# Kernel optimization log

Hardware: AMD Instinct MI355X
Metric: run time of the kernel (lower is better)

Reference implementation:

```python
import jax, jax.numpy as jnp
import numpy as np

NUM_CLASSES = 19
PROJ_DIM = 128
QUEUE_LEN = 2975
B, H, W = 8, 128, 128
EPS = 1e-12  # torch F.normalize eps


def setup_inputs() -> dict:
    key = jax.random.key(0)
    k0, k1, k2, k3, k4 = jax.random.split(key, 5)
    proj3 = jax.random.normal(k0, (B, PROJ_DIM, H, W), jnp.float32)
    proj4 = jax.random.normal(k1, (B, PROJ_DIM, H, W), jnp.float32)
    proj5 = jax.random.normal(k2, (B, PROJ_DIM, H, W), jnp.float32)
    logits = jax.random.normal(k3, (B, NUM_CLASSES, H, W), jnp.float32)
    q = jax.random.normal(k4, (3, NUM_CLASSES, PROJ_DIM, QUEUE_LEN), jnp.float32)
    # buffers are L2-normalized along proj_dim at init
    queues = q / jnp.maximum(jnp.linalg.norm(q, axis=2, keepdims=True), EPS)
    return {"proj3": proj3, "proj4": proj4, "proj5": proj5,
            "logits": logits, "queues": queues}


def _region_keys(fea, pred):
    """fea: (D, HW) float, pred: (HW,) int. Masked mean per class, L2-normalized."""
    onehot = (pred[None, :] == jnp.arange(NUM_CLASSES)[:, None]).astype(fea.dtype)  # (C, HW)
    counts = onehot.sum(1)                                   # (C,)
    sums = jnp.einsum('ch,dh->cd', onehot, fea)              # (C, D)
    present = counts > 0
    means = sums / jnp.maximum(counts, 1.0)[:, None]
    keys = means / jnp.maximum(jnp.linalg.norm(means, axis=1, keepdims=True), EPS)
    return keys, present


def _contrast_loss(keys, present, queue):
    """keys: (C, D), queue: (C, D, L) (detached in original). Sum over present classes."""
    q = jax.lax.stop_gradient(queue)
    # (query . queue_col) implemented as elementwise-mul + mean over D in the original
    sim = jnp.einsum('cd,kdl->ckl', keys, q) / PROJ_DIM      # (C, C, L)
    ar = jnp.arange(NUM_CLASSES)
    pos = sim[ar, ar, :]                                     # (C, L)  l_pos per class
    exp_all = jnp.exp(sim)
    s_neg = exp_all.sum(axis=(1, 2)) - exp_all[ar, ar, :].sum(1)  # scalar neg mass per class
    loss_c = -(pos - jnp.log(jnp.exp(pos) + s_neg[:, None])).sum(1) / QUEUE_LEN
    return jnp.where(present, loss_c, 0.0).sum()


def _enqueue(queue, ptr, keys, present):
    """Write key into queue column ptr[c] for present classes, advance ptr by 1."""
    ar = jnp.arange(NUM_CLASSES)
    cur = queue[ar, :, ptr]                                  # (C, D)
    newcol = jnp.where(present[:, None], jax.lax.stop_gradient(keys), cur)
    queue = queue.at[ar, :, ptr].set(newcol)
    ptr = jnp.where(present, (ptr + 1) % QUEUE_LEN, ptr)
    return queue, ptr


def reference(proj3, proj4, proj5, logits, queues):
    pred = jnp.argmax(logits, axis=1).reshape(B, -1)         # (B, HW)
    total = jnp.float32(0.0)
    for pi, projector in enumerate((proj3, proj4, proj5)):
        fea_all = projector.reshape(B, PROJ_DIM, -1)          # (B, D, HW)

        def step(carry, inp):
            queue, ptr, acc = carry
            f, p = inp
            keys, present = _region_keys(f, p)
            acc = acc + _contrast_loss(keys, present, queue)
            queue, ptr = _enqueue(queue, ptr, keys, present)
            return (queue, ptr, acc), None

        init = (queues[pi], jnp.zeros((NUM_CLASSES,), jnp.int32), jnp.float32(0.0))
        (_, _, acc), _ = jax.lax.scan(step, init, (fea_all, pred))
        total = total + acc / B
    return total
```

## Files before the change

### kernel.cpp

```cpp
#include <hip/hip_runtime.h>
#include <stdint.h>

#define NCLS 19
#define PDIM 128
#define QLEN 2975
#define BATCH 8
#define HW 16384
#define ROWS 152
#define ROWS_PAD 160
#define HCHUNK 512

typedef __attribute__((ext_vector_type(8))) short short8;
typedef __attribute__((ext_vector_type(4))) float floatx4;

__device__ __forceinline__ uint16_t f2b(float f) {
    uint32_t u = __float_as_uint(f);
    uint32_t r = (u + 0x7FFFu + ((u >> 16) & 1u)) >> 16;
    return (uint16_t)r;
}

__global__ __launch_bounds__(256)
void k_pred(const float* __restrict__ logits, uint8_t* __restrict__ pred,
            int* __restrict__ counts) {
    __shared__ int cnt[NCLS];
    int tid = threadIdx.x;
    if (tid < NCLS) cnt[tid] = 0;
    __syncthreads();
    int idx = blockIdx.x * 256 + tid;
    int b = idx >> 14, h = idx & (HW - 1);
    const float* base = logits + (size_t)b * NCLS * HW + h;
    float best = base[0];
    int bi = 0;
#pragma unroll
    for (int c = 1; c < NCLS; ++c) {
        float v = base[(size_t)c * HW];
        if (v > best) { best = v; bi = c; }
    }
    pred[idx] = (uint8_t)bi;
    atomicAdd(&cnt[bi], 1);
    __syncthreads();
    if (tid < NCLS) atomicAdd(&counts[b * NCLS + tid], cnt[tid]);
}

__global__ __launch_bounds__(512)
void k_msum(const float* __restrict__ p0, const float* __restrict__ p1,
            const float* __restrict__ p2, const uint8_t* __restrict__ pred,
            float* __restrict__ sums) {
    int chunk = blockIdx.x, b = blockIdx.y, pi = blockIdx.z;
    const float* proj = (pi == 0) ? p0 : (pi == 1) ? p1 : p2;
    int tid = threadIdx.x;
    int wave = tid >> 6, lane = tid & 63;
    int col = lane & 15, g = lane >> 4;
    int d = wave * 16 + col;
    int h0 = chunk * HCHUNK;

    const float* frow = proj + ((size_t)b * PDIM + d) * HW;
    const uint8_t* pr = pred + (size_t)b * HW + h0;

    floatx4 acc0 = (floatx4)(0.f);
    floatx4 acc1 = (floatx4)(0.f);

#pragma unroll 4
    for (int s = 0; s < HCHUNK / 32; ++s) {
        int hk = h0 + s * 32 + g * 8;
        union { float4 f; uint4 u; } va, vb;
        va.f = *(const float4*)(frow + hk);
        vb.f = *(const float4*)(frow + hk + 4);
        uint64_t pb = *(const uint64_t*)(pr + s * 32 + g * 8);

        union { short8 s8; uint32_t w[4]; } bf;
        bf.w[0] = __builtin_amdgcn_perm(va.u.y, va.u.x, 0x07060302u);
        bf.w[1] = __builtin_amdgcn_perm(va.u.w, va.u.z, 0x07060302u);
        bf.w[2] = __builtin_amdgcn_perm(vb.u.y, vb.u.x, 0x07060302u);
        bf.w[3] = __builtin_amdgcn_perm(vb.u.w, vb.u.z, 0x07060302u);

        union { short8 s8; uint16_t h[8]; } a0, a1;
#pragma unroll
        for (int j = 0; j < 8; ++j) {
            int cb = (int)((pb >> (8 * j)) & 0xFF);
            a0.h[j] = (cb == col)      ? (uint16_t)0x3F80 : (uint16_t)0;
            a1.h[j] = (cb == col + 16) ? (uint16_t)0x3F80 : (uint16_t)0;
        }
        acc0 = __builtin_amdgcn_mfma_f32_16x16x32_bf16(a0.s8, bf.s8, acc0, 0, 0, 0);
        acc1 = __builtin_amdgcn_mfma_f32_16x16x32_bf16(a1.s8, bf.s8, acc1, 0, 0, 0);
    }

    float* sb = sums + (((size_t)pi * BATCH + b) * NCLS) * PDIM + d;
#pragma unroll
    for (int r = 0; r < 4; ++r) {
        int row0 = g * 4 + r;
        atomicAdd(&sb[(size_t)row0 * PDIM], acc0[r]);
        int row1 = 16 + g * 4 + r;
        if (row1 < NCLS) atomicAdd(&sb[(size_t)row1 * PDIM], acc1[r]);
    }
}

__global__ __launch_bounds__(64)
void k_keys(const float* __restrict__ sums, const int* __restrict__ counts,
            uint16_t* __restrict__ keysb) {
    int c = blockIdx.x, b = blockIdx.y, pi = blockIdx.z;
    int lane = threadIdx.x;
    size_t base = (((size_t)pi * BATCH + b) * NCLS + c) * PDIM;
    int cn = counts[b * NCLS + c];
    float cnt = (float)(cn > 0 ? cn : 1);
    float m0 = sums[base + lane] / cnt;
    float m1 = sums[base + lane + 64] / cnt;
    float nr = m0 * m0 + m1 * m1;
    for (int off = 32; off; off >>= 1) nr += __shfl_xor(nr, off);
    float scale = 1.f / fmaxf(sqrtf(nr), 1e-12f);
    size_t bb = ((size_t)pi * ROWS_PAD + b * NCLS + c) * PDIM;
    keysb[bb + lane]      = f2b(m0 * scale);
    keysb[bb + lane + 64] = f2b(m1 * scale);
}

__global__ __launch_bounds__(256, 2)
void k_sim(const float* __restrict__ q, const uint16_t* __restrict__ keysb,
           float* __restrict__ Sall, float* __restrict__ D0,
           float* __restrict__ pos0) {
    __shared__ char smem[40960];
    int tile = blockIdx.x, k = blockIdx.y, pi = blockIdx.z;
    int tid = threadIdx.x;
    int wave = tid >> 6, lane = tid & 63;
    int col = lane & 15, g = lane >> 4;

    {
        const uint4* kg = (const uint4*)(keysb + (size_t)pi * ROWS_PAD * PDIM);
        uint4* kl = (uint4*)smem;
        int kgrp = tid & 15;
        int r0 = tid >> 4;
#pragma unroll
        for (int it = 0; it < 10; ++it) {
            int row = r0 + it * 16;
            kl[kgrp * 160 + (row ^ (kgrp & 7))] = kg[row * 16 + kgrp];
        }
    }

    int l0 = tile * 128 + wave * 16 + col;
    int l1 = l0 + 64;
    bool okA = l0 < QLEN, okB = l1 < QLEN;
    const uint32_t* qbase = (const uint32_t*)(q + ((size_t)pi * NCLS + k) * (size_t)PDIM * QLEN);
    const uint32_t* qA = qbase + (okA ? l0 : (QLEN - 1));
    const uint32_t* qB = qbase + (okB ? l1 : (QLEN - 1));

    uint32_t uA[32], uB[32];
#pragma unroll
    for (int s = 0; s < 4; ++s) {
#pragma unroll
        for (int j = 0; j < 8; ++j) {
            size_t off = (size_t)(s * 32 + g * 8 + j) * QLEN;
            uA[s * 8 + j] = qA[off];
            uB[s * 8 + j] = qB[off];
        }
    }

    __syncthreads();

    uint32_t wA[16], wB[16];
#pragma unroll
    for (int t = 0; t < 16; ++t) {
        wA[t] = __builtin_amdgcn_perm(uA[2 * t + 1], uA[2 * t], 0x07060302u);
        wB[t] = __builtin_amdgcn_perm(uB[2 * t + 1], uB[2 * t], 0x07060302u);
    }

    floatx4 accA[10], accB[10];
#pragma unroll
    for (int m = 0; m < 10; ++m) { accA[m] = (floatx4)(0.f); accB[m] = (floatx4)(0.f); }

    const short8* kls = (const short8*)smem;
#pragma unroll
    for (int s = 0; s < 4; ++s) {
        union { short8 s8; uint32_t w[4]; } bfA, bfB;
#pragma unroll
        for (int i = 0; i < 4; ++i) { bfA.w[i] = wA[s * 4 + i]; bfB.w[i] = wB[s * 4 + i]; }
        int kgrp = s * 4 + g;
        int kxor = kgrp & 7;
        const short8* kp = kls + (size_t)kgrp * 160;
#pragma unroll
        for (int m = 0; m < 10; ++m) {
            short8 af = kp[(m * 16 + col) ^ kxor];
            accA[m] = __builtin_amdgcn_mfma_f32_16x16x32_bf16(af, bfA.s8, accA[m], 0, 0, 0);
            accB[m] = __builtin_amdgcn_mfma_f32_16x16x32_bf16(af, bfB.s8, accB[m], 0, 0, 0);
        }
    }

    __syncthreads();
    float* rowsum = (float*)smem;
    if (tid < ROWS_PAD) rowsum[tid] = 0.f;
    __syncthreads();

    const float inv = 1.f / (float)PDIM;
#pragma unroll
    for (int m = 0; m < 10; ++m) {
#pragma unroll
        for (int r = 0; r < 4; ++r) {
            int row = m * 16 + g * 4 + r;
            bool rok = row < ROWS;
            float sA = accA[m][r] * inv;
            float sB = accB[m][r] * inv;
            float e = 0.f;
            if (rok) e = (okA ? __expf(sA) : 0.f) + (okB ? __expf(sB) : 0.f);
#pragma unroll
            for (int off = 1; off < 16; off <<= 1) e += __shfl_xor(e, off);
            if (col == 0 && rok) atomicAdd(&rowsum[row], e);
            if (rok) {
                int bb = row / NCLS, cc = row - bb * NCLS;
                if (cc == k) {
                    float* pb = pos0 + (((size_t)pi * BATCH + bb) * NCLS + cc) * QLEN;
                    if (okA) pb[l0] = sA;
                    if (okB) pb[l1] = sB;
                }
            }
        }
    }
    __syncthreads();
    if (tid < ROWS) {
        float v = rowsum[tid];
        atomicAdd(&Sall[pi * ROWS + tid], v);
        int cc = tid % NCLS;
        if (cc == k) atomicAdd(&D0[pi * ROWS + tid], v);
    }
}

__global__ __launch_bounds__(256)
void k_loss(const float* __restrict__ pos0, const float* __restrict__ Sall,
            const float* __restrict__ D0, const int* __restrict__ counts,
            float* __restrict__ out) {
    int c = blockIdx.x, b = blockIdx.y, pi = blockIdx.z;
    if (counts[b * NCLS + c] <= 0) return;
    int tid = threadIdx.x;
    int row = b * NCLS + c;
    float sneg = Sall[pi * ROWS + row] - D0[pi * ROWS + row];
    const float* pp = pos0 + (((size_t)pi * BATCH + b) * NCLS + c) * QLEN;
    float sum = 0.f;
    for (int l = tid; l < QLEN; l += 256) {
        float p = pp[l];
        sum += p - logf(__expf(p) + sneg);
    }
    __shared__ float red[4];
    int wave = tid >> 6, lane = tid & 63;
    for (int off = 32; off; off >>= 1) sum += __shfl_down(sum, off);
    if (lane == 0) red[wave] = sum;
    __syncthreads();
    if (tid == 0) {
        float t = red[0] + red[1] + red[2] + red[3];
        atomicAdd(out, -t / ((float)QLEN * (float)BATCH));
    }
}

extern "C" void kernel_launch(void* const* d_in, const int* in_sizes, int n_in,
                              void* d_out, int out_size, void* d_ws, size_t ws_size,
                              hipStream_t stream) {
    const float* proj3  = (const float*)d_in[0];
    const float* proj4  = (const float*)d_in[1];
    const float* proj5  = (const float*)d_in[2];
    const float* logits = (const float*)d_in[3];
    const float* queues = (const float*)d_in[4];

    char* ws = (char*)d_ws;
    int*      counts = (int*)ws;
    uint8_t*  pred   = (uint8_t*)(ws + 1024);
    float*    sums   = (float*)(ws + 1024 + 131072);
    uint16_t* keysb  = (uint16_t*)(ws + 365568);
    float*    Sall   = (float*)(ws + 488448);
    float*    D0f    = (float*)(ws + 490496);
    float*    pos0   = (float*)(ws + 492544);

    hipMemsetAsync(ws, 0, 492544, stream);
    hipMemsetAsync(d_out, 0, sizeof(float), stream);

    k_pred<<<dim3(512), 256, 0, stream>>>(logits, pred, counts);

    dim3 gs(32, BATCH, 3);
    k_msum<<<gs, 512, 0, stream>>>(proj3, proj4, proj5, pred, sums);

    dim3 gk(NCLS, BATCH, 3);
    k_keys<<<gk, 64, 0, stream>>>(sums, counts, keysb);

    dim3 gm((QLEN + 127) / 128, NCLS, 3);
    k_sim<<<gm, 256, 0, stream>>>(queues, keysb, Sall, D0f, pos0);

    dim3 gl(NCLS, BATCH, 3);
    k_loss<<<gl, 256, 0, stream>>>(pos0, Sall, D0f, counts, (float*)d_out);
}
```

Before: 127.6 us.

## Compute proj4/proj5 class sums in fp32 with a scalar per-row kernel

The fused masked-sum kernel is split in two. Projector 3 keeps the bf16 MFMA one-hot path. Projectors 4 and 5 get a new kernel that streams each (batch, dim) row and accumulates 19 fp32 per-class sums in registers, then reduces them across waves and applies them with atomics. This looks aimed at accuracy, or at trying a different split between the two paths, and it adds per-element compare/select work plus an extra launch.

```diff
diff --git a/kernel.cpp b/kernel.cpp
--- a/kernel.cpp
+++ b/kernel.cpp
@@ -43,11 +43,9 @@
 }
 
 __global__ __launch_bounds__(512)
-void k_msum(const float* __restrict__ p0, const float* __restrict__ p1,
-            const float* __restrict__ p2, const uint8_t* __restrict__ pred,
-            float* __restrict__ sums) {
-    int chunk = blockIdx.x, b = blockIdx.y, pi = blockIdx.z;
-    const float* proj = (pi == 0) ? p0 : (pi == 1) ? p1 : p2;
+void k_msA(const float* __restrict__ proj, const uint8_t* __restrict__ pred,
+           float* __restrict__ sums) {
+    int chunk = blockIdx.x, b = blockIdx.y;
     int tid = threadIdx.x;
     int wave = tid >> 6, lane = tid & 63;
     int col = lane & 15, g = lane >> 4;
@@ -85,13 +83,68 @@
         acc1 = __builtin_amdgcn_mfma_f32_16x16x32_bf16(a1.s8, bf.s8, acc1, 0, 0, 0);
     }
 
-    float* sb = sums + (((size_t)pi * BATCH + b) * NCLS) * PDIM + d;
+    float* sb = sums + ((size_t)b * NCLS) * PDIM + d;
 #pragma unroll
     for (int r = 0; r < 4; ++r) {
         int row0 = g * 4 + r;
         atomicAdd(&sb[(size_t)row0 * PDIM], acc0[r]);
         int row1 = 16 + g * 4 + r;
         if (row1 < NCLS) atomicAdd(&sb[(size_t)row1 * PDIM], acc1[r]);
+    }
+}
+
+__global__ __launch_bounds__(256)
+void k_msB(const float* __restrict__ p1, const float* __restrict__ p2,
+           const uint8_t* __restrict__ pred, float* __restrict__ sums) {
+    int which = blockIdx.y;
+    const float* proj = which ? p2 : p1;
+    int pi = which + 1;
+    int tid = threadIdx.x;
+    int half = tid >> 7, t = tid & 127;
+    int row = blockIdx.x * 2 + half;
+    int b = row >> 7, d = row & 127;
+
+    const float4* src = (const float4*)(proj + (size_t)row * HW);
+    const uint32_t* pr = (const uint32_t*)(pred + (size_t)b * HW);
+
+    float acc[NCLS];
+#pragma unroll
+    for (int c = 0; c < NCLS; ++c) acc[c] = 0.f;
+
+#pragma unroll 4
+    for (int j = 0; j < 32; ++j) {
+        float4 v = src[j * 128 + t];
+        uint32_t pc = pr[j * 128 + t];
+        float ve;
+        int p;
+#pragma unroll
+        for (int e = 0; e < 4; ++e) {
+            ve = (e == 0) ? v.x : (e == 1) ? v.y : (e == 2) ? v.z : v.w;
+            p = (int)((pc >> (8 * e)) & 0xFFu);
+#pragma unroll
+            for (int c = 0; c < NCLS; ++c)
+                acc[c] += (p == c) ? ve : 0.f;
+        }
+    }
+
+    __shared__ float red[4][NCLS];
+    int wave = tid >> 6, lane = tid & 63;
+#pragma unroll
+    for (int c = 0; c < NCLS; ++c) {
+        float v = acc[c];
+        for (int off = 32; off; off >>= 1) v += __shfl_down(v, off);
+        if (lane == 0) red[wave][c] = v;
+    }
+    __syncthreads();
+    if (tid < NCLS) {
+        float s = red[0][tid] + red[1][tid];
+        int r0 = blockIdx.x * 2, b0 = r0 >> 7, d0 = r0 & 127;
+        atomicAdd(&sums[(((size_t)pi * BATCH + b0) * NCLS + tid) * PDIM + d0], s);
+    } else if (tid >= 128 && tid < 128 + NCLS) {
+        int c = tid - 128;
+        float s = red[2][c] + red[3][c];
+        int r1 = blockIdx.x * 2 + 1, b1 = r1 >> 7, d1 = r1 & 127;
+        atomicAdd(&sums[(((size_t)pi * BATCH + b1) * NCLS + c) * PDIM + d1], s);
     }
 }
 
@@ -270,8 +323,10 @@
 
     k_pred<<<dim3(512), 256, 0, stream>>>(logits, pred, counts);
 
-    dim3 gs(32, BATCH, 3);
-    k_msum<<<gs, 512, 0, stream>>>(proj3, proj4, proj5, pred, sums);
+    dim3 ga(32, BATCH);
+    k_msA<<<ga, 512, 0, stream>>>(proj3, pred, sums);
+    dim3 gb(512, 2);
+    k_msB<<<gb, 256, 0, stream>>>(proj4, proj5, pred, sums);
 
     dim3 gk(NCLS, BATCH, 3);
     k_keys<<<gk, 64, 0, stream>>>(sums, counts, keysb);
```

Result: slower. 168.3 us (+31.9%).

## Double-buffer k_msum loads with inline asm and split D across smaller blocks

Applied to the files above, without the earlier changes.

Rewrites the masked-sum kernel to issue batches of global loads through inline asm into two register buffers, with explicit vmcnt waits so the MFMA work on one buffer overlaps the loads for the next. Each block now covers half the projection dims with 256 threads, doubling the grid, and an occupancy hint is added. In k_sim, sched barriers plus empty asm uses force all queue loads to be issued before the syncthreads. The goal is to hide memory latency on a bandwidth-bound reduction, at the cost of higher register pressure and fragile hand-written asm.

```diff
diff --git a/kernel.cpp b/kernel.cpp
--- a/kernel.cpp
+++ b/kernel.cpp
@@ -8,16 +8,62 @@
 #define HW 16384
 #define ROWS 152
 #define ROWS_PAD 160
-#define HCHUNK 512
 
 typedef __attribute__((ext_vector_type(8))) short short8;
 typedef __attribute__((ext_vector_type(4))) float floatx4;
+typedef __attribute__((ext_vector_type(4))) unsigned int uint32x4;
+
+#define KEEPU32(u)  asm volatile("" :: "v"(u))
 
 __device__ __forceinline__ uint16_t f2b(float f) {
     uint32_t u = __float_as_uint(f);
     uint32_t r = (u + 0x7FFFu + ((u >> 16) & 1u)) >> 16;
     return (uint16_t)r;
 }
+
+#define LOADB(va, vb, pb, fbp, ppp)                                        \
+  asm volatile(                                                            \
+    "global_load_dwordx4 %0, %8, off\n\t"                                  \
+    "global_load_dwordx4 %1, %8, off offset:128\n\t"                       \
+    "global_load_dwordx4 %2, %8, off offset:256\n\t"                       \
+    "global_load_dwordx4 %3, %8, off offset:384\n\t"                       \
+    "global_load_dwordx4 %4, %8, off offset:16\n\t"                        \
+    "global_load_dwordx4 %5, %8, off offset:144\n\t"                       \
+    "global_load_dwordx4 %6, %8, off offset:272\n\t"                       \
+    "global_load_dwordx4 %7, %8, off offset:400\n\t"                       \
+    : "=&v"(va[0]), "=&v"(va[1]), "=&v"(va[2]), "=&v"(va[3]),              \
+      "=&v"(vb[0]), "=&v"(vb[1]), "=&v"(vb[2]), "=&v"(vb[3])               \
+    : "v"(fbp));                                                           \
+  asm volatile(                                                            \
+    "global_load_dwordx2 %0, %4, off\n\t"                                  \
+    "global_load_dwordx2 %1, %4, off offset:32\n\t"                        \
+    "global_load_dwordx2 %2, %4, off offset:64\n\t"                        \
+    "global_load_dwordx2 %3, %4, off offset:96\n\t"                        \
+    : "=&v"(pb[0]), "=&v"(pb[1]), "=&v"(pb[2]), "=&v"(pb[3])               \
+    : "v"(ppp))
+
+#define WAITC(N)                                                           \
+  asm volatile("s_waitcnt vmcnt(" #N ")" ::: "memory");                    \
+  __builtin_amdgcn_sched_barrier(0)
+
+#define CONSUME(va, vb, pb)                                                \
+  _Pragma("unroll")                                                        \
+  for (int s = 0; s < 4; ++s) {                                            \
+    union { short8 s8; uint32_t w[4]; } bf;                                \
+    bf.w[0] = __builtin_amdgcn_perm(va[s][1], va[s][0], 0x07060302u);      \
+    bf.w[1] = __builtin_amdgcn_perm(va[s][3], va[s][2], 0x07060302u);      \
+    bf.w[2] = __builtin_amdgcn_perm(vb[s][1], vb[s][0], 0x07060302u);      \
+    bf.w[3] = __builtin_amdgcn_perm(vb[s][3], vb[s][2], 0x07060302u);      \
+    union { short8 s8; uint16_t h[8]; } a0, a1;                            \
+    _Pragma("unroll")                                                      \
+    for (int j = 0; j < 8; ++j) {                                          \
+      int cb = (int)((pb[s] >> (8 * j)) & 0xFF);                           \
+      a0.h[j] = (cb == col)      ? (uint16_t)0x3F80 : (uint16_t)0;         \
+      a1.h[j] = (cb == col + 16) ? (uint16_t)0x3F80 : (uint16_t)0;         \
+    }                                                                      \
+    acc0 = __builtin_amdgcn_mfma_f32_16x16x32_bf16(a0.s8, bf.s8, acc0, 0, 0, 0); \
+    acc1 = __builtin_amdgcn_mfma_f32_16x16x32_bf16(a1.s8, bf.s8, acc1, 0, 0, 0); \
+  }
 
 __global__ __launch_bounds__(256)
 void k_pred(const float* __restrict__ logits, uint8_t* __restrict__ pred,
@@ -42,48 +88,42 @@
     if (tid < NCLS) atomicAdd(&counts[b * NCLS + tid], cnt[tid]);
 }
 
-__global__ __launch_bounds__(512)
+__global__ __launch_bounds__(256, 4)
 void k_msum(const float* __restrict__ p0, const float* __restrict__ p1,
             const float* __restrict__ p2, const uint8_t* __restrict__ pred,
             float* __restrict__ sums) {
-    int chunk = blockIdx.x, b = blockIdx.y, pi = blockIdx.z;
+    int cx = blockIdx.x;
+    int chunk = cx >> 1, dq = cx & 1;
+    int b = blockIdx.y, pi = blockIdx.z;
     const float* proj = (pi == 0) ? p0 : (pi == 1) ? p1 : p2;
     int tid = threadIdx.x;
     int wave = tid >> 6, lane = tid & 63;
     int col = lane & 15, g = lane >> 4;
-    int d = wave * 16 + col;
-    int h0 = chunk * HCHUNK;
-
-    const float* frow = proj + ((size_t)b * PDIM + d) * HW;
-    const uint8_t* pr = pred + (size_t)b * HW + h0;
+    int d = dq * 64 + wave * 16 + col;
+
+    const char* fb = (const char*)(proj + ((size_t)b * PDIM + d) * HW
+                                   + (size_t)chunk * 512) + g * 32;
+    const char* pp = (const char*)(pred + (size_t)b * HW + chunk * 512) + g * 8;
+
+    uint32x4 vaA[4], vbA[4]; uint64_t pbA[4];
+    uint32x4 vaB[4], vbB[4]; uint64_t pbB[4];
+
+    LOADB(vaA, vbA, pbA, fb, pp);
+    LOADB(vaB, vbB, pbB, fb + 512, pp + 128);
 
     floatx4 acc0 = (floatx4)(0.f);
     floatx4 acc1 = (floatx4)(0.f);
 
-#pragma unroll 4
-    for (int s = 0; s < HCHUNK / 32; ++s) {
-        int hk = h0 + s * 32 + g * 8;
-        union { float4 f; uint4 u; } va, vb;
-        va.f = *(const float4*)(frow + hk);
-        vb.f = *(const float4*)(frow + hk + 4);
-        uint64_t pb = *(const uint64_t*)(pr + s * 32 + g * 8);
-
-        union { short8 s8; uint32_t w[4]; } bf;
-        bf.w[0] = __builtin_amdgcn_perm(va.u.y, va.u.x, 0x07060302u);
-        bf.w[1] = __builtin_amdgcn_perm(va.u.w, va.u.z, 0x07060302u);
-        bf.w[2] = __builtin_amdgcn_perm(vb.u.y, vb.u.x, 0x07060302u);
-        bf.w[3] = __builtin_amdgcn_perm(vb.u.w, vb.u.z, 0x07060302u);
-
-        union { short8 s8; uint16_t h[8]; } a0, a1;
-#pragma unroll
-        for (int j = 0; j < 8; ++j) {
-            int cb = (int)((pb >> (8 * j)) & 0xFF);
-            a0.h[j] = (cb == col)      ? (uint16_t)0x3F80 : (uint16_t)0;
-            a1.h[j] = (cb == col + 16) ? (uint16_t)0x3F80 : (uint16_t)0;
-        }
-        acc0 = __builtin_amdgcn_mfma_f32_16x16x32_bf16(a0.s8, bf.s8, acc0, 0, 0, 0);
-        acc1 = __builtin_amdgcn_mfma_f32_16x16x32_bf16(a1.s8, bf.s8, acc1, 0, 0, 0);
-    }
+    WAITC(12);
+    CONSUME(vaA, vbA, pbA);
+    LOADB(vaA, vbA, pbA, fb + 1024, pp + 256);
+    WAITC(12);
+    CONSUME(vaB, vbB, pbB);
+    LOADB(vaB, vbB, pbB, fb + 1536, pp + 384);
+    WAITC(12);
+    CONSUME(vaA, vbA, pbA);
+    WAITC(0);
+    CONSUME(vaB, vbB, pbB);
 
     float* sb = sums + (((size_t)pi * BATCH + b) * NCLS) * PDIM + d;
 #pragma unroll
@@ -152,6 +192,10 @@
             uB[s * 8 + j] = qB[off];
         }
     }
+    __builtin_amdgcn_sched_barrier(0);
+#pragma unroll
+    for (int i = 0; i < 32; ++i) { KEEPU32(uA[i]); KEEPU32(uB[i]); }
+    __builtin_amdgcn_sched_barrier(0);
 
     __syncthreads();
 
@@ -270,8 +314,8 @@
 
     k_pred<<<dim3(512), 256, 0, stream>>>(logits, pred, counts);
 
-    dim3 gs(32, BATCH, 3);
-    k_msum<<<gs, 512, 0, stream>>>(proj3, proj4, proj5, pred, sums);
+    dim3 gs(64, BATCH, 3);
+    k_msum<<<gs, 256, 0, stream>>>(proj3, proj4, proj5, pred, sums);
 
     dim3 gk(NCLS, BATCH, 3);
     k_keys<<<gk, 64, 0, stream>>>(sums, counts, keysb);
```

New measurement: 129.6 us. Within noise of the previous version (+1.6%).
